# Kernel optimization log

Measured on AMD Instinct MI355X. Metric: run time of the kernel, lower is better.

Reference implementation:

```python
import jax, jax.numpy as jnp
import numpy as np

K = 5  # filter_size (matches init_kwargs)


def _adaptive_pool_matrix(size: int, k: int) -> jnp.ndarray:
    """Row-stochastic [k, size] matrix replicating torch adaptive_avg_pool1d bins."""
    P = np.zeros((k, size), np.float32)
    for i in range(k):
        s = (i * size) // k
        e = -((-(i + 1) * size) // k)  # ceil((i+1)*size/k)
        P[i, s:e] = 1.0 / (e - s)
    return jnp.asarray(P)


def setup_inputs() -> dict:
    key = jax.random.key(0)
    k1, k2, k3 = jax.random.split(key, 3)
    B, Cin, Cout, H, W = 8, 32, 32, 256, 256
    x = jax.random.normal(k1, (B, Cin, H, W), jnp.float32)
    conv_w = jax.random.normal(k2, (Cout, Cin), jnp.float32) * (1.0 / np.sqrt(Cin))
    conv_b = jax.random.normal(k3, (Cout,), jnp.float32) * 0.01
    return {"x": x, "conv_w": conv_w, "conv_b": conv_b}


def reference(x, conv_w, conv_b):
    B, Cin, H, W = x.shape
    # 1x1 conv == channel-mixing einsum
    feat = jnp.einsum('bihw,oi->bohw', x, conv_w) + conv_b[None, :, None, None]
    C = feat.shape[1]
    # adaptive_avg_pool2d(feat, K) via static pooling matrices -> per-(b,c) KxK filter
    Ph = _adaptive_pool_matrix(H, K)
    Pw = _adaptive_pool_matrix(W, K)
    filt = jnp.einsum('kh,bchw,lw->bckl', Ph, feat, Pw)  # [B, C, K, K]
    # pad per original intent ('same' output), then grouped conv with groups=B*C
    pad = (K - 1) // 2
    if (K - 1) % 2 == 0:
        p = ((pad, pad), (pad, pad))
    else:
        p = ((pad + 1, pad), (pad + 1, pad))
    inp = feat.reshape(1, B * C, H, W)
    w = filt.reshape(B * C, 1, K, K)
    out = jax.lax.conv_general_dilated(
        inp, w, window_strides=(1, 1), padding=p,
        dimension_numbers=('NCHW', 'OIHW', 'NCHW'),
        feature_group_count=B * C)
    return out.reshape(B, C, H, W)
```

## Files before the change

### kernel.cpp

```cpp
#include <hip/hip_runtime.h>


#define CIN 32
#define COUT 32
#define HW 256
#define PLANE (HW * HW)
#define BATCH 8
#define KF 5
#define BIN 52

__global__ __launch_bounds__(256) void conv1x1_pool_kernel(const float* __restrict__ x,
                                                           const float* __restrict__ Wm,
                                                           const float* __restrict__ bias,
                                                           float* __restrict__ feat,
                                                           float* __restrict__ filt_raw) {
    int b   = blockIdx.x >> 8;
    int row = blockIdx.x & 255;
    int t   = threadIdx.x;

    const float* xb = x + (size_t)b * CIN * PLANE + row * HW + t;

    float acc[COUT];
#pragma unroll
    for (int o = 0; o < COUT; ++o) acc[o] = bias[o];

#pragma unroll
    for (int ig = 0; ig < 4; ++ig) {
        float xv[8];
#pragma unroll
        for (int j = 0; j < 8; ++j) xv[j] = xb[(size_t)(ig * 8 + j) * PLANE];
#pragma unroll
        for (int o = 0; o < COUT; ++o) {
#pragma unroll
            for (int j = 0; j < 8; ++j)
                acc[o] += Wm[o * CIN + ig * 8 + j] * xv[j];
        }
    }

    float* fb = feat + (size_t)b * COUT * PLANE + row * HW + t;
#pragma unroll
    for (int o = 0; o < COUT; ++o) fb[(size_t)o * PLANE] = acc[o];

    __shared__ float lds[COUT * HW];
#pragma unroll
    for (int o = 0; o < COUT; ++o) lds[o * HW + t] = acc[o];
    __syncthreads();

    if (t < COUT * KF) {
        int o  = t / KF;
        int l  = t - o * KF;
        int sl = (l * HW) / KF;
        float s = 0.f;
        for (int w = 0; w < BIN; ++w) s += lds[o * HW + sl + w];
        float* dst = filt_raw + (size_t)(b * COUT + o) * 25 + l;
#pragma unroll
        for (int k = 0; k < KF; ++k) {
            int sk = (k * HW) / KF;
            if (row >= sk && row < sk + BIN) atomicAdd(dst + k * KF, s);
        }
    }
}

#define LROW 264
#define STRIP 16
__global__ __launch_bounds__(256) void dwconv_kernel(const float* __restrict__ feat,
                                                     const float* __restrict__ filt_raw,
                                                     float* __restrict__ out) {
    int bo    = blockIdx.y;
    int strip = blockIdx.x;
    int gy0   = strip * STRIP;
    int t     = threadIdx.x;

    __shared__ __align__(16) float s[(STRIP + 4) * LROW];
    __shared__ float sfilt[25];
    if (t < 25) sfilt[t] = filt_raw[bo * 25 + t] * (1.0f / (52.0f * 52.0f));
    if (t < 160) {
        int lr = t >> 3, e = t & 7;
        int ci = (e < 4) ? e : (256 + e);
        s[lr * LROW + ci] = 0.f;
    }

    const float* fb = feat + (size_t)bo * PLANE;
#pragma unroll
    for (int j = 0; j < 5; ++j) {
        int idx = t + 256 * j;
        int lr  = idx >> 6;
        int cx  = (idx & 63) * 4;
        int gy  = gy0 - 2 + lr;
        float4 v = {0.f, 0.f, 0.f, 0.f};
        if ((unsigned)gy < (unsigned)HW) v = *(const float4*)(fb + gy * HW + cx);
        *(float4*)(&s[lr * LROW + 4 + cx]) = v;
    }
    __syncthreads();

    float fw[25];
#pragma unroll
    for (int j = 0; j < 25; ++j) fw[j] = sfilt[j];

    int cg  = t & 127;
    int rq  = t >> 7;
    int lr0 = rq * 8;
    int ci0 = 2 * cg + 2;

    float w[5][6];
#pragma unroll
    for (int r = 0; r < 4; ++r) {
        const float* rp = &s[(lr0 + r) * LROW + ci0];
        float2 a = *(const float2*)(rp);
        float2 c = *(const float2*)(rp + 2);
        float2 e = *(const float2*)(rp + 4);
        w[r][0] = a.x; w[r][1] = a.y; w[r][2] = c.x;
        w[r][3] = c.y; w[r][4] = e.x; w[r][5] = e.y;
    }

    float* ob = out + (size_t)bo * PLANE + (size_t)(gy0 + 8 * rq) * HW + 2 * cg;
#pragma unroll
    for (int r = 0; r < 8; ++r) {
        const float* rp = &s[(lr0 + r + 4) * LROW + ci0];
        float2 a = *(const float2*)(rp);
        float2 c = *(const float2*)(rp + 2);
        float2 e = *(const float2*)(rp + 4);
        w[4][0] = a.x; w[4][1] = a.y; w[4][2] = c.x;
        w[4][3] = c.y; w[4][4] = e.x; w[4][5] = e.y;

        float a0 = 0.f, a1 = 0.f;
#pragma unroll
        for (int kh = 0; kh < 5; ++kh) {
#pragma unroll
            for (int j = 0; j < 5; ++j) {
                float wv = fw[kh * 5 + j];
                a0 += wv * w[kh][j];
                a1 += wv * w[kh][j + 1];
            }
        }
        *(float2*)(ob + r * HW) = make_float2(a0, a1);

#pragma unroll
        for (int kh = 0; kh < 4; ++kh)
#pragma unroll
            for (int j = 0; j < 6; ++j) w[kh][j] = w[kh + 1][j];
    }
}

extern "C" void kernel_launch(void* const* d_in, const int* in_sizes, int n_in,
                              void* d_out, int out_size, void* d_ws, size_t ws_size,
                              hipStream_t stream) {
    const float* x      = (const float*)d_in[0];
    const float* conv_w = (const float*)d_in[1];
    const float* conv_b = (const float*)d_in[2];
    float* out = (float*)d_out;

    float* feat = (float*)d_ws;
    float* filt = feat + (size_t)BATCH * COUT * PLANE;

    hipMemsetAsync(filt, 0, BATCH * COUT * 25 * sizeof(float), stream);
    conv1x1_pool_kernel<<<dim3(BATCH * 256), dim3(256), 0, stream>>>(x, conv_w, conv_b, feat, filt);
    dwconv_kernel<<<dim3(STRIP, BATCH * COUT), dim3(256), 0, stream>>>(feat, filt, out);
}
```

Before: 158.4 us.

## Retile conv1x1 by row and output-channel groups with float4 and widen dwconv strips

The conv1x1+pool kernel now gives each block 4 rows and 8 output channels, with each thread computing 4 adjacent pixels via float4 loads and stores. This cuts per-thread accumulator registers and vectorises memory access, at the cost of reading x four times, once per channel group. The depthwise conv kernel now processes 32-row strips, with each thread producing 4 columns × 8 rows. That reduces the halo overhead and the redundant shared-memory loads per output, in exchange for more LDS and registers per block and fewer blocks.

```diff
diff --git a/kernel.cpp b/kernel.cpp
--- a/kernel.cpp
+++ b/kernel.cpp
@@ -9,80 +9,96 @@
 #define KF 5
 #define BIN 52
 
+#define PROW 260
 __global__ __launch_bounds__(256) void conv1x1_pool_kernel(const float* __restrict__ x,
                                                            const float* __restrict__ Wm,
                                                            const float* __restrict__ bias,
                                                            float* __restrict__ feat,
                                                            float* __restrict__ filt_raw) {
     int b   = blockIdx.x >> 8;
-    int row = blockIdx.x & 255;
+    int rem = blockIdx.x & 255;
+    int rg  = rem >> 2;
+    int og  = rem & 3;
+    int r0  = rg * 4, o0 = og * 8;
     int t   = threadIdx.x;
+    int rp  = t >> 6;
+    int c0  = (t & 63) * 4;
+    int row = r0 + rp;
 
-    const float* xb = x + (size_t)b * CIN * PLANE + row * HW + t;
+    const float* xb = x + (size_t)b * CIN * PLANE + row * HW + c0;
 
-    float acc[COUT];
+    float4 acc[8];
 #pragma unroll
-    for (int o = 0; o < COUT; ++o) acc[o] = bias[o];
+    for (int oo = 0; oo < 8; ++oo) {
+        float bv = bias[o0 + oo];
+        acc[oo].x = bv; acc[oo].y = bv; acc[oo].z = bv; acc[oo].w = bv;
+    }
 
 #pragma unroll
-    for (int ig = 0; ig < 4; ++ig) {
-        float xv[8];
+    for (int ig = 0; ig < 8; ++ig) {
+        float4 xv[4];
 #pragma unroll
-        for (int j = 0; j < 8; ++j) xv[j] = xb[(size_t)(ig * 8 + j) * PLANE];
+        for (int j = 0; j < 4; ++j) xv[j] = *(const float4*)(xb + (size_t)(ig * 4 + j) * PLANE);
 #pragma unroll
-        for (int o = 0; o < COUT; ++o) {
+        for (int oo = 0; oo < 8; ++oo) {
 #pragma unroll
-            for (int j = 0; j < 8; ++j)
-                acc[o] += Wm[o * CIN + ig * 8 + j] * xv[j];
+            for (int j = 0; j < 4; ++j) {
+                float wv = Wm[(o0 + oo) * CIN + ig * 4 + j];
+                acc[oo].x += wv * xv[j].x; acc[oo].y += wv * xv[j].y;
+                acc[oo].z += wv * xv[j].z; acc[oo].w += wv * xv[j].w;
+            }
         }
     }
 
-    float* fb = feat + (size_t)b * COUT * PLANE + row * HW + t;
+    float* fb = feat + ((size_t)b * COUT + o0) * PLANE + row * HW + c0;
 #pragma unroll
-    for (int o = 0; o < COUT; ++o) fb[(size_t)o * PLANE] = acc[o];
+    for (int oo = 0; oo < 8; ++oo) *(float4*)(fb + (size_t)oo * PLANE) = acc[oo];
 
-    __shared__ float lds[COUT * HW];
+    __shared__ __align__(16) float lds[8 * 4 * PROW];
 #pragma unroll
-    for (int o = 0; o < COUT; ++o) lds[o * HW + t] = acc[o];
+    for (int oo = 0; oo < 8; ++oo)
+        *(float4*)(&lds[(oo * 4 + rp) * PROW + c0]) = acc[oo];
     __syncthreads();
 
-    if (t < COUT * KF) {
-        int o  = t / KF;
-        int l  = t - o * KF;
+    if (t < 160) {
+        int oo = t / 20;
+        int rr = (t / 5) % 4;
+        int l  = t % 5;
         int sl = (l * HW) / KF;
+        const float* lp = &lds[(oo * 4 + rr) * PROW + sl];
         float s = 0.f;
-        for (int w = 0; w < BIN; ++w) s += lds[o * HW + sl + w];
-        float* dst = filt_raw + (size_t)(b * COUT + o) * 25 + l;
+        for (int w = 0; w < BIN; ++w) s += lp[w];
+        int row2 = r0 + rr;
+        float* dst = filt_raw + (size_t)(b * COUT + o0 + oo) * 25 + l;
 #pragma unroll
         for (int k = 0; k < KF; ++k) {
             int sk = (k * HW) / KF;
-            if (row >= sk && row < sk + BIN) atomicAdd(dst + k * KF, s);
+            if (row2 >= sk && row2 < sk + BIN) atomicAdd(dst + k * KF, s);
         }
     }
 }
 
 #define LROW 264
-#define STRIP 16
 __global__ __launch_bounds__(256) void dwconv_kernel(const float* __restrict__ feat,
                                                      const float* __restrict__ filt_raw,
                                                      float* __restrict__ out) {
     int bo    = blockIdx.y;
     int strip = blockIdx.x;
-    int gy0   = strip * STRIP;
+    int gy0   = strip * 32;
     int t     = threadIdx.x;
 
-    __shared__ __align__(16) float s[(STRIP + 4) * LROW];
+    __shared__ __align__(16) float s[36 * LROW];
     __shared__ float sfilt[25];
     if (t < 25) sfilt[t] = filt_raw[bo * 25 + t] * (1.0f / (52.0f * 52.0f));
-    if (t < 160) {
-        int lr = t >> 3, e = t & 7;
+    for (int idx = t; idx < 288; idx += 256) {
+        int lr = idx >> 3, e = idx & 7;
         int ci = (e < 4) ? e : (256 + e);
         s[lr * LROW + ci] = 0.f;
     }
 
     const float* fb = feat + (size_t)bo * PLANE;
 #pragma unroll
-    for (int j = 0; j < 5; ++j) {
+    for (int j = 0; j < 9; ++j) {
         int idx = t + 256 * j;
         int lr  = idx >> 6;
         int cx  = (idx & 63) * 4;
@@ -97,48 +113,50 @@
 #pragma unroll
     for (int j = 0; j < 25; ++j) fw[j] = sfilt[j];
 
-    int cg  = t & 127;
-    int rq  = t >> 7;
+    int cq  = t & 63;
+    int rq  = t >> 6;
     int lr0 = rq * 8;
-    int ci0 = 2 * cg + 2;
+    int ci0 = 4 * cq + 2;
 
-    float w[5][6];
+    float w[5][8];
 #pragma unroll
     for (int r = 0; r < 4; ++r) {
         const float* rp = &s[(lr0 + r) * LROW + ci0];
-        float2 a = *(const float2*)(rp);
-        float2 c = *(const float2*)(rp + 2);
-        float2 e = *(const float2*)(rp + 4);
-        w[r][0] = a.x; w[r][1] = a.y; w[r][2] = c.x;
-        w[r][3] = c.y; w[r][4] = e.x; w[r][5] = e.y;
+#pragma unroll
+        for (int j = 0; j < 4; ++j) {
+            float2 v = *(const float2*)(rp + 2 * j);
+            w[r][2 * j] = v.x; w[r][2 * j + 1] = v.y;
+        }
     }
 
-    float* ob = out + (size_t)bo * PLANE + (size_t)(gy0 + 8 * rq) * HW + 2 * cg;
+    float* ob = out + (size_t)bo * PLANE + (size_t)(gy0 + 8 * rq) * HW + 4 * cq;
 #pragma unroll
     for (int r = 0; r < 8; ++r) {
         const float* rp = &s[(lr0 + r + 4) * LROW + ci0];
-        float2 a = *(const float2*)(rp);
-        float2 c = *(const float2*)(rp + 2);
-        float2 e = *(const float2*)(rp + 4);
-        w[4][0] = a.x; w[4][1] = a.y; w[4][2] = c.x;
-        w[4][3] = c.y; w[4][4] = e.x; w[4][5] = e.y;
+#pragma unroll
+        for (int j = 0; j < 4; ++j) {
+            float2 v = *(const float2*)(rp + 2 * j);
+            w[4][2 * j] = v.x; w[4][2 * j + 1] = v.y;
+        }
 
-        float a0 = 0.f, a1 = 0.f;
+        float4 a = {0.f, 0.f, 0.f, 0.f};
 #pragma unroll
         for (int kh = 0; kh < 5; ++kh) {
 #pragma unroll
             for (int j = 0; j < 5; ++j) {
                 float wv = fw[kh * 5 + j];
-                a0 += wv * w[kh][j];
-                a1 += wv * w[kh][j + 1];
+                a.x += wv * w[kh][j];
+                a.y += wv * w[kh][j + 1];
+                a.z += wv * w[kh][j + 2];
+                a.w += wv * w[kh][j + 3];
             }
         }
-        *(float2*)(ob + r * HW) = make_float2(a0, a1);
+        *(float4*)(ob + r * HW) = a;
 
 #pragma unroll
         for (int kh = 0; kh < 4; ++kh)
 #pragma unroll
-            for (int j = 0; j < 6; ++j) w[kh][j] = w[kh + 1][j];
+            for (int j = 0; j < 8; ++j) w[kh][j] = w[kh + 1][j];
     }
 }
 
@@ -155,5 +173,5 @@
 
     hipMemsetAsync(filt, 0, BATCH * COUT * 25 * sizeof(float), stream);
     conv1x1_pool_kernel<<<dim3(BATCH * 256), dim3(256), 0, stream>>>(x, conv_w, conv_b, feat, filt);
-    dwconv_kernel<<<dim3(STRIP, BATCH * COUT), dim3(256), 0, stream>>>(feat, filt, out);
+    dwconv_kernel<<<dim3(8, BATCH * COUT), dim3(256), 0, stream>>>(feat, filt, out);
 }
```

Measured after the change: 175.8 us. 10.9% more time.
